# Kernel optimization log

Measured on AMD Instinct MI355X. Metric: run time of the kernel, lower is better.

Reference implementation:

```python
import jax, jax.numpy as jnp
import numpy as np

N = 50000   # nodes
E = 600000  # directed edges (self-loops added inside reference, per GCNConv default)
G = 64      # graphs in the batch
D = 128     # in_features
H = 128     # hidden_channels
C = 10      # num_classes


def setup_inputs() -> dict:
    key = jax.random.key(0)
    ks = jax.random.split(key, 9)
    x = jax.random.normal(ks[0], (N, D), dtype=jnp.float32)
    edge_index = jax.random.randint(ks[1], (2, E), 0, N, dtype=jnp.int64)
    batch = jnp.sort(jax.random.randint(ks[2], (N,), 0, G, dtype=jnp.int64))
    # GCNConv weights (glorot-ish scale) and biases; final linear layer
    W1 = jax.random.normal(ks[3], (D, H), dtype=jnp.float32) / np.sqrt(D).astype(np.float32)
    b1 = jnp.zeros((H,), dtype=jnp.float32)
    W2 = jax.random.normal(ks[4], (H, H), dtype=jnp.float32) / np.sqrt(H).astype(np.float32)
    b2 = jnp.zeros((H,), dtype=jnp.float32)
    Wlin = jax.random.normal(ks[5], (H, C), dtype=jnp.float32) / np.sqrt(H).astype(np.float32)
    blin = jnp.zeros((C,), dtype=jnp.float32)
    return {"x": x, "W1": W1, "b1": b1, "W2": W2, "b2": b2,
            "Wlin": Wlin, "blin": blin, "edge_index": edge_index, "batch": batch}


def _gcn_conv(x, W, b, row, col, norm):
    # x' = D^{-1/2}(A+I)D^{-1/2} (x W) + b ; aggregate messages from row (src) into col (dst)
    h = x @ W                                   # [N, H] dense GEMM
    msg = norm[:, None] * h[row]                # gather by source index [E+N, H]
    out = jax.ops.segment_sum(msg, col, num_segments=N)  # scatter-add to targets
    return out + b


def reference(x, W1, b1, W2, b2, Wlin, blin, edge_index, batch):
    loops = jnp.arange(N, dtype=edge_index.dtype)
    row = jnp.concatenate([edge_index[0], loops])   # sources (+ self loops)
    col = jnp.concatenate([edge_index[1], loops])   # targets (+ self loops)
    # symmetric degree normalization (degrees >= 1 thanks to self loops)
    deg = jax.ops.segment_sum(jnp.ones_like(col, dtype=jnp.float32), col, num_segments=N)
    dinv = jax.lax.rsqrt(deg)
    norm = dinv[row] * dinv[col]                    # [E+N]

    h = jax.nn.relu(_gcn_conv(x, W1, b1, row, col, norm))
    h = _gcn_conv(h, W2, b2, row, col, norm)

    # global mean pool over graphs
    sums = jax.ops.segment_sum(h, batch, num_segments=G)                       # [G, H]
    cnt = jax.ops.segment_sum(jnp.ones((N,), dtype=jnp.float32), batch, num_segments=G)
    pooled = sums / jnp.maximum(cnt, 1.0)[:, None]

    return pooled @ Wlin + blin                     # logits [G, C]
```

## Files before the change

kernel.cpp:

```cpp
#include <hip/hip_runtime.h>

#define NN 50000
#define NE 600000
#define NG 64
#define DIM 128
#define NCLS 10
#define SB 196
#define NNP 50176
#define KBLK 392
#define KCH 128
#define CAP 64
#define E2B ((NE / 2 + 255) / 256)
#define BSW_TAIL_START ((size_t)(NN >> 5) * 4096)

typedef unsigned short ushort;
typedef unsigned char uchar;
typedef __attribute__((ext_vector_type(8))) short short8;
typedef __attribute__((ext_vector_type(4))) float float4v;
typedef __attribute__((ext_vector_type(2))) float float2v;

__device__ __forceinline__ ushort f2bf(float f) {
    unsigned u = __float_as_uint(f);
    u += 0x7fff + ((u >> 16) & 1);
    return (ushort)(u >> 16);
}
__device__ __forceinline__ uchar f2fp8(float f) {
    int p = __builtin_amdgcn_cvt_pk_fp8_f32(f, f, 0, false);
    return (uchar)(p & 0xff);
}
__device__ __forceinline__ void accfp8(float* a, uint2 v) {
    float2v p0 = __builtin_amdgcn_cvt_pk_f32_fp8(v.x, false);
    float2v p1 = __builtin_amdgcn_cvt_pk_f32_fp8(v.x, true);
    float2v p2 = __builtin_amdgcn_cvt_pk_f32_fp8(v.y, false);
    float2v p3 = __builtin_amdgcn_cvt_pk_f32_fp8(v.y, true);
    a[0] += p0[0]; a[1] += p0[1]; a[2] += p1[0]; a[3] += p1[1];
    a[4] += p2[0]; a[5] += p2[1]; a[6] += p3[0]; a[7] += p3[1];
}

__global__ void k_init(int* __restrict__ cnt, const float* __restrict__ W1,
                       ushort* __restrict__ Wsw, float* __restrict__ T,
                       float* __restrict__ dinv, ushort* __restrict__ Bsw) {
    int b = blockIdx.x, t = threadIdx.x;
    if (b < SB) {
        int i = b * 256 + t;
        if (i < NN) cnt[i] = 0;
    } else if (b < SB + 64) {
        int tid = (b - SB) * 256 + t;
        int j = tid & 7;
        int lane = (tid >> 3) & 63;
        int frag = tid >> 9;
        int nt = frag >> 2, kc = frag & 3;
        int k = kc * 32 + (lane >> 4) * 8 + j;
        int n = nt * 16 + (lane & 15);
        Wsw[tid] = f2bf(W1[k * DIM + n]);
    } else if (b < SB + 64 + 784) {
        float4* w4 = (float4*)T;
        int base = (b - SB - 64) * 256 + t;
#pragma unroll
        for (int i = 0; i < 4; ++i)
            w4[base + i * 200704] = make_float4(0.f, 0.f, 0.f, 0.f);
    } else if (b == SB + 64 + 784) {
        if (t < NNP - NN) dinv[NN + t] = 0.f;
    } else {
        int idx = (b - (SB + 64 + 785)) * 256 + t;
        ((float4*)(Bsw + BSW_TAIL_START))[idx] = make_float4(0.f, 0.f, 0.f, 0.f);
    }
}

__global__ void k_fill(const int* __restrict__ row, const int* __restrict__ col,
                       int* __restrict__ cnt, ushort* __restrict__ ell) {
    int e = (blockIdx.x * blockDim.x + threadIdx.x) * 2;
    if (e < NE) {
        int2 r = *(const int2*)(row + e);
        int2 c = *(const int2*)(col + e);
        int p0 = atomicAdd(&cnt[c.x], 1);
        if (p0 < CAP) ell[(size_t)c.x * CAP + p0] = (ushort)r.x;
        int p1 = atomicAdd(&cnt[c.y], 1);
        if (p1 < CAP) ell[(size_t)c.y * CAP + p1] = (ushort)r.y;
    }
}

__global__ __launch_bounds__(256) void k_gemm_mfma(const float* __restrict__ Ain,
                                                   const ushort* __restrict__ Wsw,
                                                   const int* __restrict__ cnt,
                                                   uchar* __restrict__ Hs,
                                                   float* __restrict__ dinv) {
    const int t = threadIdx.x;
    const int wave = t >> 6, lane = t & 63;
    const int m = lane & 15, quad = lane >> 4;
    const int row0 = blockIdx.x * 64 + wave * 16;

    short8 bfrag[8][4];
#pragma unroll
    for (int nt = 0; nt < 8; ++nt)
#pragma unroll
        for (int kc = 0; kc < 4; ++kc)
            bfrag[nt][kc] = *(const short8*)(Wsw + ((nt * 4 + kc) * 64 + lane) * 8);

    float4v acc[8];
#pragma unroll
    for (int nt = 0; nt < 8; ++nt) acc[nt] = (float4v){0.f, 0.f, 0.f, 0.f};

    const int row = row0 + m;
    const int rclamp = row < NN ? row : NN - 1;

#pragma unroll
    for (int kc = 0; kc < 4; ++kc) {
        const float* ap = Ain + (size_t)rclamp * DIM + kc * 32 + quad * 8;
        float4 v0 = *(const float4*)ap;
        float4 v1 = *(const float4*)(ap + 4);
        union { short8 v; ushort u[8]; } tmp;
        tmp.u[0] = f2bf(v0.x); tmp.u[1] = f2bf(v0.y);
        tmp.u[2] = f2bf(v0.z); tmp.u[3] = f2bf(v0.w);
        tmp.u[4] = f2bf(v1.x); tmp.u[5] = f2bf(v1.y);
        tmp.u[6] = f2bf(v1.z); tmp.u[7] = f2bf(v1.w);
        short8 a = tmp.v;
#pragma unroll
        for (int nt = 0; nt < 8; ++nt)
            acc[nt] = __builtin_amdgcn_mfma_f32_16x16x32_bf16(a, bfrag[nt][kc], acc[nt], 0, 0, 0);
    }

#pragma unroll
    for (int reg = 0; reg < 4; ++reg) {
        int r = row0 + quad * 4 + reg;
        if (r < NN) {
            float d = rsqrtf(1.0f + (float)cnt[r]);
            if (m == 0) dinv[r] = d;
#pragma unroll
            for (int nt = 0; nt < 8; ++nt)
                Hs[(size_t)r * DIM + nt * 16 + m] = f2fp8(d * acc[nt][reg]);
        }
    }
}

__global__ __launch_bounds__(256) void k_gather_ell(const ushort* __restrict__ ell,
                                                    const int* __restrict__ deg,
                                                    const int* __restrict__ batch,
                                                    const float* __restrict__ bias,
                                                    const uchar* __restrict__ Hs,
                                                    float* __restrict__ T,
                                                    ushort* __restrict__ Bsw) {
    const int t = threadIdx.x, b = blockIdx.x;
    const int tn = t >> 4, lane = t & 15;
    const int node = b * 16 + tn;
    const ushort* rowp = ell + (size_t)node * CAP;
    int end = min(deg[node], CAP);
    const float d = rsqrtf(1.0f + (float)end);
    float* Trow = T + (size_t)batch[node] * NNP;
    const size_t off = (size_t)lane * 8;

    float a[8] = {0.f, 0.f, 0.f, 0.f, 0.f, 0.f, 0.f, 0.f};
    accfp8(a, *(const uint2*)(Hs + (size_t)node * DIM + off));
    if (lane == 0) atomicAdd(&Trow[node], d);

    int e = 0;
    for (; e + 8 <= end; e += 8) {
        uint4 iv = *(const uint4*)(rowp + e);
        int r0 = iv.x & 0xffff, r1 = iv.x >> 16;
        int r2 = iv.y & 0xffff, r3 = iv.y >> 16;
        int r4 = iv.z & 0xffff, r5 = iv.z >> 16;
        int r6 = iv.w & 0xffff, r7 = iv.w >> 16;
        if (lane < 8) atomicAdd(&Trow[rowp[e + lane]], d);
        uint2 v0 = *(const uint2*)(Hs + (size_t)r0 * DIM + off);
        uint2 v1 = *(const uint2*)(Hs + (size_t)r1 * DIM + off);
        uint2 v2 = *(const uint2*)(Hs + (size_t)r2 * DIM + off);
        uint2 v3 = *(const uint2*)(Hs + (size_t)r3 * DIM + off);
        uint2 v4 = *(const uint2*)(Hs + (size_t)r4 * DIM + off);
        uint2 v5 = *(const uint2*)(Hs + (size_t)r5 * DIM + off);
        uint2 v6 = *(const uint2*)(Hs + (size_t)r6 * DIM + off);
        uint2 v7 = *(const uint2*)(Hs + (size_t)r7 * DIM + off);
        accfp8(a, v0); accfp8(a, v1); accfp8(a, v2); accfp8(a, v3);
        accfp8(a, v4); accfp8(a, v5); accfp8(a, v6); accfp8(a, v7);
    }
    for (; e + 4 <= end; e += 4) {
        uint2 lv = *(const uint2*)(rowp + e);
        int r0 = lv.x & 0xffff, r1 = lv.x >> 16;
        int r2 = lv.y & 0xffff, r3 = lv.y >> 16;
        if (lane < 4) atomicAdd(&Trow[rowp[e + lane]], d);
        uint2 v0 = *(const uint2*)(Hs + (size_t)r0 * DIM + off);
        uint2 v1 = *(const uint2*)(Hs + (size_t)r1 * DIM + off);
        uint2 v2 = *(const uint2*)(Hs + (size_t)r2 * DIM + off);
        uint2 v3 = *(const uint2*)(Hs + (size_t)r3 * DIM + off);
        accfp8(a, v0); accfp8(a, v1); accfp8(a, v2); accfp8(a, v3);
    }
    for (; e < end; ++e) {
        int r = rowp[e];
        if (lane == 0) atomicAdd(&Trow[r], d);
        accfp8(a, *(const uint2*)(Hs + (size_t)r * DIM + off));
    }

    float4 b0 = *(const float4*)(bias + off);
    float4 b1 = *(const float4*)(bias + off + 4);
    a[0] = fmaxf(fmaf(a[0], d, b0.x), 0.f); a[1] = fmaxf(fmaf(a[1], d, b0.y), 0.f);
    a[2] = fmaxf(fmaf(a[2], d, b0.z), 0.f); a[3] = fmaxf(fmaf(a[3], d, b0.w), 0.f);
    a[4] = fmaxf(fmaf(a[4], d, b1.x), 0.f); a[5] = fmaxf(fmaf(a[5], d, b1.y), 0.f);
    a[6] = fmaxf(fmaf(a[6], d, b1.z), 0.f); a[7] = fmaxf(fmaf(a[7], d, b1.w), 0.f);

    __shared__ ushort Lb[16][128];
    union { short8 v; ushort u[8]; } st;
    st.u[0] = f2bf(a[0]); st.u[1] = f2bf(a[1]); st.u[2] = f2bf(a[2]); st.u[3] = f2bf(a[3]);
    st.u[4] = f2bf(a[4]); st.u[5] = f2bf(a[5]); st.u[6] = f2bf(a[6]); st.u[7] = f2bf(a[7]);
    *(short8*)(&Lb[tn][lane * 8]) = st.v;
    __syncthreads();

    const int nt = t >> 5, idx = t & 31;
    const int a_rel = (idx >> 4) & 1, fb = (idx >> 3) & 1, f7 = idx & 7;
    const int feat = nt * 16 + fb * 8 + f7;
    const int nl = a_rel * 8;
    uint4 o;
    o.x = (unsigned)Lb[nl + 0][feat] | ((unsigned)Lb[nl + 1][feat] << 16);
    o.y = (unsigned)Lb[nl + 2][feat] | ((unsigned)Lb[nl + 3][feat] << 16);
    o.z = (unsigned)Lb[nl + 4][feat] | ((unsigned)Lb[nl + 5][feat] << 16);
    o.w = (unsigned)Lb[nl + 6][feat] | ((unsigned)Lb[nl + 7][feat] << 16);
    size_t base = (size_t)(b >> 1) * 4096 + (size_t)nt * 512
                + (size_t)((b & 1) * 2 + a_rel) * 128 + (size_t)fb * 64 + (size_t)f7 * 8;
    *(uint4*)(Bsw + base) = o;
}

__global__ __launch_bounds__(256) void k_pool_gemm(const float* __restrict__ T,
                                                   const float* __restrict__ dinv,
                                                   const ushort* __restrict__ Bsw,
                                                   float* __restrict__ partial) {
    const int t = threadIdx.x;
    const int wave = t >> 6, lane = t & 63;
    const int m = lane & 15, quad = lane >> 4;
    const int g = wave * 16 + m;
    const int k0 = blockIdx.x * KCH;

    float4v acc[8];
#pragma unroll
    for (int nt = 0; nt < 8; ++nt) acc[nt] = (float4v){0.f, 0.f, 0.f, 0.f};

#pragma unroll
    for (int s = 0; s < KCH / 32; ++s) {
        const int kb = k0 + s * 32 + quad * 8;
        const float* ap = T + (size_t)g * NNP + kb;
        float4 a0 = *(const float4*)ap;
        float4 a1 = *(const float4*)(ap + 4);
        float4 d0 = *(const float4*)(dinv + kb);
        float4 d1 = *(const float4*)(dinv + kb + 4);
        union { short8 v; ushort u[8]; } af;
        af.u[0] = f2bf(a0.x * d0.x); af.u[1] = f2bf(a0.y * d0.y);
        af.u[2] = f2bf(a0.z * d0.z); af.u[3] = f2bf(a0.w * d0.w);
        af.u[4] = f2bf(a1.x * d1.x); af.u[5] = f2bf(a1.y * d1.y);
        af.u[6] = f2bf(a1.z * d1.z); af.u[7] = f2bf(a1.w * d1.w);

        const int t32 = (k0 >> 5) + s;
        const ushort* bb = Bsw + (size_t)t32 * 4096 + (size_t)lane * 8;
#pragma unroll
        for (int nt = 0; nt < 8; ++nt) {
            short8 bv = *(const short8*)(bb + nt * 512);
            acc[nt] = __builtin_amdgcn_mfma_f32_16x16x32_bf16(af.v, bv, acc[nt], 0, 0, 0);
        }
    }

    float* dst = partial + (size_t)blockIdx.x * (NG * DIM);
#pragma unroll
    for (int reg = 0; reg < 4; ++reg) {
        int gg = wave * 16 + quad * 4 + reg;
#pragma unroll
        for (int nt = 0; nt < 8; ++nt)
            dst[gg * DIM + nt * 16 + m] = acc[nt][reg];
    }
}

__global__ __launch_bounds__(512) void k_final(const float* __restrict__ partial,
                                               const float* __restrict__ W2,
                                               const float* __restrict__ b2,
                                               const float* __restrict__ Wlin,
                                               const float* __restrict__ blin,
                                               const int* __restrict__ batch,
                                               float* __restrict__ out) {
    const int g = blockIdx.x;
    const int t = threadIdx.x;
    const int c = t & 127, h = t >> 7;

    float s0 = 0.f, s1 = 0.f;
    const float* pp = partial + (size_t)h * 98 * (NG * DIM) + g * DIM + c;
#pragma unroll 7
    for (int i = 0; i < 98; i += 2) {
        s0 += pp[(size_t)i * (NG * DIM)];
        s1 += pp[(size_t)(i + 1) * (NG * DIM)];
    }

    __shared__ float red[512];
    __shared__ float Pl[DIM];
    __shared__ float pooled[DIM];
    red[t] = s0 + s1;
    __syncthreads();
    if (t < 128) Pl[t] = red[t] + red[t + 128] + red[t + 256] + red[t + 384];
    __syncthreads();
    if (t < 128) {
        float acc = 0.f;
        for (int k = 0; k < DIM; ++k) acc += Pl[k] * W2[k * DIM + t];
        int start;
        { int a = 0, bb = NN; while (a < bb) { int mm = (a + bb) >> 1; if (batch[mm] < g) a = mm + 1; else bb = mm; } start = a; }
        int endp;
        { int a = 0, bb = NN; while (a < bb) { int mm = (a + bb) >> 1; if (batch[mm] < g + 1) a = mm + 1; else bb = mm; } endp = a; }
        const int cnt = endp - start;
        pooled[t] = (cnt > 0) ? (acc / (float)cnt + b2[t]) : 0.f;
    }
    __syncthreads();
    if (t < NCLS) {
        float s2 = blin[t];
        for (int k = 0; k < DIM; ++k) s2 += pooled[k] * Wlin[k * NCLS + t];
        out[g * NCLS + t] = s2;
    }
}

extern "C" void kernel_launch(void* const* d_in, const int* in_sizes, int n_in,
                              void* d_out, int out_size, void* d_ws, size_t ws_size,
                              hipStream_t stream) {
    const float* x    = (const float*)d_in[0];
    const float* W1   = (const float*)d_in[1];
    const float* b1   = (const float*)d_in[2];
    const float* W2   = (const float*)d_in[3];
    const float* b2   = (const float*)d_in[4];
    const float* Wlin = (const float*)d_in[5];
    const float* blin = (const float*)d_in[6];
    const int* eidx   = (const int*)d_in[7];
    const int* batch  = (const int*)d_in[8];
    float* out = (float*)d_out;

    char* ws = (char*)d_ws;
    int*    cnt   = (int*)(ws + 0);
    float*  dinv  = (float*)(ws + 200000);
    ushort* Wsw   = (ushort*)(ws + 400704);
    ushort* ell   = (ushort*)(ws + 433472);
    uchar*  Hs1   = (uchar*)(ws + 6833472);
    float*  T     = (float*)(ws + 13233472);
    ushort* Bsw   = (ushort*)(ws + 26078528);
    float*  partial=(float*)(ws + 38923584);

    const int* erow = eidx;
    const int* ecol = eidx + NE;

    k_init<<<SB + 64 + 784 + 1 + 12, 256, 0, stream>>>(cnt, W1, Wsw, T, dinv, Bsw);
    k_fill<<<E2B, 256, 0, stream>>>(erow, ecol, cnt, ell);

    const int gemm_grid = (NN + 63) / 64;
    const int node_grid = NN / 16;

    k_gemm_mfma<<<gemm_grid, 256, 0, stream>>>(x, Wsw, cnt, Hs1, dinv);
    k_gather_ell<<<node_grid, 256, 0, stream>>>(ell, cnt, batch, b1, Hs1, T, Bsw);

    k_pool_gemm<<<KBLK, 256, 0, stream>>>(T, dinv, Bsw, partial);

    k_final<<<NG, 512, 0, stream>>>(partial, W2, b2, Wlin, blin, batch, out);
}
```

Measured before the change: 198.6 us.

## Count degrees early and overlap ELL fill with first-layer GEMM in one kernel

Degree counting moves into the init kernel, interleaved with zeroing T, so the GEMM can apply the dinv scaling without waiting for the ELL fill. The fill and GEMM are then merged into one launch whose blocks alternate roles, letting the atomic-heavy fill overlap the MFMA work. Alongside this, dinv scaling is folded into the gather epilogue so the pool GEMM no longer reads dinv, the gather loop is software-prefetched one batch of 8 neighbours ahead, and the final partial reduction is split into a separate atomic reduce kernel. The cost is an extra memset, a second counter array and one more kernel launch.

```diff
diff --git a/kernel.cpp b/kernel.cpp
--- a/kernel.cpp
+++ b/kernel.cpp
@@ -5,12 +5,15 @@
 #define NG 64
 #define DIM 128
 #define NCLS 10
-#define SB 196
 #define NNP 50176
 #define KBLK 392
 #define KCH 128
 #define CAP 64
-#define E2B ((NE / 2 + 255) / 256)
+#define FILLB 1172
+#define GEMMB 782
+#define PAIR (GEMMB * 2)
+#define TZB 784
+#define IPAIR (TZB * 2)
 #define BSW_TAIL_START ((size_t)(NN >> 5) * 4096)
 
 typedef unsigned short ushort;
@@ -36,16 +39,37 @@
     a[0] += p0[0]; a[1] += p0[1]; a[2] += p1[0]; a[3] += p1[1];
     a[4] += p2[0]; a[5] += p2[1]; a[6] += p3[0]; a[7] += p3[1];
 }
-
-__global__ void k_init(int* __restrict__ cnt, const float* __restrict__ W1,
-                       ushort* __restrict__ Wsw, float* __restrict__ T,
-                       float* __restrict__ dinv, ushort* __restrict__ Bsw) {
+__device__ __forceinline__ uint2 ldrow(const uchar* __restrict__ Hs, int r, size_t off) {
+    return *(const uint2*)(Hs + (size_t)r * DIM + off);
+}
+
+__global__ void k_init(const int* __restrict__ ecol, int* __restrict__ cnt,
+                       const float* __restrict__ W1, ushort* __restrict__ Wsw,
+                       float* __restrict__ T, ushort* __restrict__ Bsw,
+                       float* __restrict__ P) {
     int b = blockIdx.x, t = threadIdx.x;
-    if (b < SB) {
-        int i = b * 256 + t;
-        if (i < NN) cnt[i] = 0;
-    } else if (b < SB + 64) {
-        int tid = (b - SB) * 256 + t;
+    int role, id;
+    if (b < IPAIR)            { role = b & 1; id = b >> 1; }
+    else if (b < IPAIR + 388) { role = 1; id = TZB + (b - IPAIR); }
+    else if (b < IPAIR + 388 + 64) { role = 2; id = b - (IPAIR + 388); }
+    else if (b < IPAIR + 388 + 64 + 12) { role = 3; id = b - (IPAIR + 388 + 64); }
+    else { role = 4; id = b - (IPAIR + 388 + 64 + 12); }
+
+    if (role == 0) {
+        float4* w4 = (float4*)T;
+        int base = id * 256 + t;
+#pragma unroll
+        for (int i = 0; i < 4; ++i)
+            w4[base + i * 200704] = make_float4(0.f, 0.f, 0.f, 0.f);
+    } else if (role == 1) {
+        int e = (id * 256 + t) * 2;
+        if (e < NE) {
+            int2 c = *(const int2*)(ecol + e);
+            atomicAdd(&cnt[c.x], 1);
+            atomicAdd(&cnt[c.y], 1);
+        }
+    } else if (role == 2) {
+        int tid = id * 256 + t;
         int j = tid & 7;
         int lane = (tid >> 3) & 63;
         int frag = tid >> 9;
@@ -53,42 +77,44 @@
         int k = kc * 32 + (lane >> 4) * 8 + j;
         int n = nt * 16 + (lane & 15);
         Wsw[tid] = f2bf(W1[k * DIM + n]);
-    } else if (b < SB + 64 + 784) {
-        float4* w4 = (float4*)T;
-        int base = (b - SB - 64) * 256 + t;
-#pragma unroll
-        for (int i = 0; i < 4; ++i)
-            w4[base + i * 200704] = make_float4(0.f, 0.f, 0.f, 0.f);
-    } else if (b == SB + 64 + 784) {
-        if (t < NNP - NN) dinv[NN + t] = 0.f;
+    } else if (role == 3) {
+        int idx = id * 256 + t;
+        ((float4*)(Bsw + BSW_TAIL_START))[idx] = make_float4(0.f, 0.f, 0.f, 0.f);
     } else {
-        int idx = (b - (SB + 64 + 785)) * 256 + t;
-        ((float4*)(Bsw + BSW_TAIL_START))[idx] = make_float4(0.f, 0.f, 0.f, 0.f);
-    }
-}
-
-__global__ void k_fill(const int* __restrict__ row, const int* __restrict__ col,
-                       int* __restrict__ cnt, ushort* __restrict__ ell) {
-    int e = (blockIdx.x * blockDim.x + threadIdx.x) * 2;
-    if (e < NE) {
-        int2 r = *(const int2*)(row + e);
-        int2 c = *(const int2*)(col + e);
-        int p0 = atomicAdd(&cnt[c.x], 1);
-        if (p0 < CAP) ell[(size_t)c.x * CAP + p0] = (ushort)r.x;
-        int p1 = atomicAdd(&cnt[c.y], 1);
-        if (p1 < CAP) ell[(size_t)c.y * CAP + p1] = (ushort)r.y;
-    }
-}
-
-__global__ __launch_bounds__(256) void k_gemm_mfma(const float* __restrict__ Ain,
-                                                   const ushort* __restrict__ Wsw,
-                                                   const int* __restrict__ cnt,
-                                                   uchar* __restrict__ Hs,
-                                                   float* __restrict__ dinv) {
-    const int t = threadIdx.x;
+        int idx = id * 256 + t;
+        ((float4*)P)[idx] = make_float4(0.f, 0.f, 0.f, 0.f);
+    }
+}
+
+__global__ __launch_bounds__(256) void k_fillgemm(const int* __restrict__ erow,
+                                                  const int* __restrict__ ecol,
+                                                  int* __restrict__ cnt2,
+                                                  ushort* __restrict__ ell,
+                                                  const float* __restrict__ Ain,
+                                                  const ushort* __restrict__ Wsw,
+                                                  const int* __restrict__ cnt,
+                                                  uchar* __restrict__ Hs) {
+    const int b = blockIdx.x, t = threadIdx.x;
+    int role, id;
+    if (b < PAIR) { role = b & 1; id = b >> 1; }
+    else          { role = 0; id = GEMMB + (b - PAIR); }
+
+    if (role == 0) {
+        int e = (id * 256 + t) * 2;
+        if (e < NE) {
+            int2 r = *(const int2*)(erow + e);
+            int2 c = *(const int2*)(ecol + e);
+            int p0 = atomicAdd(&cnt2[c.x], 1);
+            if (p0 < CAP) ell[(size_t)c.x * CAP + p0] = (ushort)r.x;
+            int p1 = atomicAdd(&cnt2[c.y], 1);
+            if (p1 < CAP) ell[(size_t)c.y * CAP + p1] = (ushort)r.y;
+        }
+        return;
+    }
+
     const int wave = t >> 6, lane = t & 63;
     const int m = lane & 15, quad = lane >> 4;
-    const int row0 = blockIdx.x * 64 + wave * 16;
+    const int row0 = id * 64 + wave * 16;
 
     short8 bfrag[8][4];
 #pragma unroll
@@ -125,7 +151,6 @@
         int r = row0 + quad * 4 + reg;
         if (r < NN) {
             float d = rsqrtf(1.0f + (float)cnt[r]);
-            if (m == 0) dinv[r] = d;
 #pragma unroll
             for (int nt = 0; nt < 8; ++nt)
                 Hs[(size_t)r * DIM + nt * 16 + m] = f2fp8(d * acc[nt][reg]);
@@ -144,49 +169,54 @@
     const int tn = t >> 4, lane = t & 15;
     const int node = b * 16 + tn;
     const ushort* rowp = ell + (size_t)node * CAP;
-    int end = min(deg[node], CAP);
-    const float d = rsqrtf(1.0f + (float)end);
+    const int dg = deg[node];
+    const float d = rsqrtf(1.0f + (float)dg);
+    const int end = min(dg, CAP);
     float* Trow = T + (size_t)batch[node] * NNP;
     const size_t off = (size_t)lane * 8;
 
     float a[8] = {0.f, 0.f, 0.f, 0.f, 0.f, 0.f, 0.f, 0.f};
-    accfp8(a, *(const uint2*)(Hs + (size_t)node * DIM + off));
+    accfp8(a, ldrow(Hs, node, off));
     if (lane == 0) atomicAdd(&Trow[node], d);
 
     int e = 0;
-    for (; e + 8 <= end; e += 8) {
-        uint4 iv = *(const uint4*)(rowp + e);
-        int r0 = iv.x & 0xffff, r1 = iv.x >> 16;
-        int r2 = iv.y & 0xffff, r3 = iv.y >> 16;
-        int r4 = iv.z & 0xffff, r5 = iv.z >> 16;
-        int r6 = iv.w & 0xffff, r7 = iv.w >> 16;
+    if (end >= 8) {
+        uint4 iv = *(const uint4*)(rowp);
+        uint2 v0 = ldrow(Hs, iv.x & 0xffff, off), v1 = ldrow(Hs, iv.x >> 16, off);
+        uint2 v2 = ldrow(Hs, iv.y & 0xffff, off), v3 = ldrow(Hs, iv.y >> 16, off);
+        uint2 v4 = ldrow(Hs, iv.z & 0xffff, off), v5 = ldrow(Hs, iv.z >> 16, off);
+        uint2 v6 = ldrow(Hs, iv.w & 0xffff, off), v7 = ldrow(Hs, iv.w >> 16, off);
+        while (e + 16 <= end) {
+            uint4 ivn = *(const uint4*)(rowp + e + 8);
+            uint2 n0 = ldrow(Hs, ivn.x & 0xffff, off), n1 = ldrow(Hs, ivn.x >> 16, off);
+            uint2 n2 = ldrow(Hs, ivn.y & 0xffff, off), n3 = ldrow(Hs, ivn.y >> 16, off);
+            uint2 n4 = ldrow(Hs, ivn.z & 0xffff, off), n5 = ldrow(Hs, ivn.z >> 16, off);
+            uint2 n6 = ldrow(Hs, ivn.w & 0xffff, off), n7 = ldrow(Hs, ivn.w >> 16, off);
+            if (lane < 8) atomicAdd(&Trow[rowp[e + lane]], d);
+            accfp8(a, v0); accfp8(a, v1); accfp8(a, v2); accfp8(a, v3);
+            accfp8(a, v4); accfp8(a, v5); accfp8(a, v6); accfp8(a, v7);
+            v0 = n0; v1 = n1; v2 = n2; v3 = n3;
+            v4 = n4; v5 = n5; v6 = n6; v7 = n7;
+            e += 8;
+        }
         if (lane < 8) atomicAdd(&Trow[rowp[e + lane]], d);
-        uint2 v0 = *(const uint2*)(Hs + (size_t)r0 * DIM + off);
-        uint2 v1 = *(const uint2*)(Hs + (size_t)r1 * DIM + off);
-        uint2 v2 = *(const uint2*)(Hs + (size_t)r2 * DIM + off);
-        uint2 v3 = *(const uint2*)(Hs + (size_t)r3 * DIM + off);
-        uint2 v4 = *(const uint2*)(Hs + (size_t)r4 * DIM + off);
-        uint2 v5 = *(const uint2*)(Hs + (size_t)r5 * DIM + off);
-        uint2 v6 = *(const uint2*)(Hs + (size_t)r6 * DIM + off);
-        uint2 v7 = *(const uint2*)(Hs + (size_t)r7 * DIM + off);
         accfp8(a, v0); accfp8(a, v1); accfp8(a, v2); accfp8(a, v3);
         accfp8(a, v4); accfp8(a, v5); accfp8(a, v6); accfp8(a, v7);
+        e += 8;
     }
     for (; e + 4 <= end; e += 4) {
         uint2 lv = *(const uint2*)(rowp + e);
         int r0 = lv.x & 0xffff, r1 = lv.x >> 16;
         int r2 = lv.y & 0xffff, r3 = lv.y >> 16;
         if (lane < 4) atomicAdd(&Trow[rowp[e + lane]], d);
-        uint2 v0 = *(const uint2*)(Hs + (size_t)r0 * DIM + off);
-        uint2 v1 = *(const uint2*)(Hs + (size_t)r1 * DIM + off);
-        uint2 v2 = *(const uint2*)(Hs + (size_t)r2 * DIM + off);
-        uint2 v3 = *(const uint2*)(Hs + (size_t)r3 * DIM + off);
-        accfp8(a, v0); accfp8(a, v1); accfp8(a, v2); accfp8(a, v3);
+        uint2 w0 = ldrow(Hs, r0, off), w1 = ldrow(Hs, r1, off);
+        uint2 w2 = ldrow(Hs, r2, off), w3 = ldrow(Hs, r3, off);
+        accfp8(a, w0); accfp8(a, w1); accfp8(a, w2); accfp8(a, w3);
     }
     for (; e < end; ++e) {
         int r = rowp[e];
         if (lane == 0) atomicAdd(&Trow[r], d);
-        accfp8(a, *(const uint2*)(Hs + (size_t)r * DIM + off));
+        accfp8(a, ldrow(Hs, r, off));
     }
 
     float4 b0 = *(const float4*)(bias + off);
@@ -198,8 +228,10 @@
 
     __shared__ ushort Lb[16][128];
     union { short8 v; ushort u[8]; } st;
-    st.u[0] = f2bf(a[0]); st.u[1] = f2bf(a[1]); st.u[2] = f2bf(a[2]); st.u[3] = f2bf(a[3]);
-    st.u[4] = f2bf(a[4]); st.u[5] = f2bf(a[5]); st.u[6] = f2bf(a[6]); st.u[7] = f2bf(a[7]);
+    st.u[0] = f2bf(d * a[0]); st.u[1] = f2bf(d * a[1]);
+    st.u[2] = f2bf(d * a[2]); st.u[3] = f2bf(d * a[3]);
+    st.u[4] = f2bf(d * a[4]); st.u[5] = f2bf(d * a[5]);
+    st.u[6] = f2bf(d * a[6]); st.u[7] = f2bf(d * a[7]);
     *(short8*)(&Lb[tn][lane * 8]) = st.v;
     __syncthreads();
 
@@ -218,7 +250,6 @@
 }
 
 __global__ __launch_bounds__(256) void k_pool_gemm(const float* __restrict__ T,
-                                                   const float* __restrict__ dinv,
                                                    const ushort* __restrict__ Bsw,
                                                    float* __restrict__ partial) {
     const int t = threadIdx.x;
@@ -237,13 +268,11 @@
         const float* ap = T + (size_t)g * NNP + kb;
         float4 a0 = *(const float4*)ap;
         float4 a1 = *(const float4*)(ap + 4);
-        float4 d0 = *(const float4*)(dinv + kb);
-        float4 d1 = *(const float4*)(dinv + kb + 4);
         union { short8 v; ushort u[8]; } af;
-        af.u[0] = f2bf(a0.x * d0.x); af.u[1] = f2bf(a0.y * d0.y);
-        af.u[2] = f2bf(a0.z * d0.z); af.u[3] = f2bf(a0.w * d0.w);
-        af.u[4] = f2bf(a1.x * d1.x); af.u[5] = f2bf(a1.y * d1.y);
-        af.u[6] = f2bf(a1.z * d1.z); af.u[7] = f2bf(a1.w * d1.w);
+        af.u[0] = f2bf(a0.x); af.u[1] = f2bf(a0.y);
+        af.u[2] = f2bf(a0.z); af.u[3] = f2bf(a0.w);
+        af.u[4] = f2bf(a1.x); af.u[5] = f2bf(a1.y);
+        af.u[6] = f2bf(a1.z); af.u[7] = f2bf(a1.w);
 
         const int t32 = (k0 >> 5) + s;
         const ushort* bb = Bsw + (size_t)t32 * 4096 + (size_t)lane * 8;
@@ -264,7 +293,18 @@
     }
 }
 
-__global__ __launch_bounds__(512) void k_final(const float* __restrict__ partial,
+__global__ __launch_bounds__(256) void k_red(const float* __restrict__ partial,
+                                             float* __restrict__ P) {
+    int tid = blockIdx.x * 256 + threadIdx.x;
+    int elem = tid & 8191, h = tid >> 13;
+    const float* pp = partial + (size_t)h * 49 * (NG * DIM) + elem;
+    float s = 0.f;
+#pragma unroll
+    for (int i = 0; i < 49; ++i) s += pp[(size_t)i * (NG * DIM)];
+    atomicAdd(&P[elem], s);
+}
+
+__global__ __launch_bounds__(128) void k_final(const float* __restrict__ P,
                                                const float* __restrict__ W2,
                                                const float* __restrict__ b2,
                                                const float* __restrict__ Wlin,
@@ -273,33 +313,19 @@
                                                float* __restrict__ out) {
     const int g = blockIdx.x;
     const int t = threadIdx.x;
-    const int c = t & 127, h = t >> 7;
-
-    float s0 = 0.f, s1 = 0.f;
-    const float* pp = partial + (size_t)h * 98 * (NG * DIM) + g * DIM + c;
-#pragma unroll 7
-    for (int i = 0; i < 98; i += 2) {
-        s0 += pp[(size_t)i * (NG * DIM)];
-        s1 += pp[(size_t)(i + 1) * (NG * DIM)];
-    }
-
-    __shared__ float red[512];
+    int start;
+    { int a = 0, bb = NN; while (a < bb) { int mm = (a + bb) >> 1; if (batch[mm] < g) a = mm + 1; else bb = mm; } start = a; }
+    int endp;
+    { int a = 0, bb = NN; while (a < bb) { int mm = (a + bb) >> 1; if (batch[mm] < g + 1) a = mm + 1; else bb = mm; } endp = a; }
+    const int cnt = endp - start;
+
     __shared__ float Pl[DIM];
     __shared__ float pooled[DIM];
-    red[t] = s0 + s1;
+    Pl[t] = P[g * DIM + t];
     __syncthreads();
-    if (t < 128) Pl[t] = red[t] + red[t + 128] + red[t + 256] + red[t + 384];
-    __syncthreads();
-    if (t < 128) {
-        float acc = 0.f;
-        for (int k = 0; k < DIM; ++k) acc += Pl[k] * W2[k * DIM + t];
-        int start;
-        { int a = 0, bb = NN; while (a < bb) { int mm = (a + bb) >> 1; if (batch[mm] < g) a = mm + 1; else bb = mm; } start = a; }
-        int endp;
-        { int a = 0, bb = NN; while (a < bb) { int mm = (a + bb) >> 1; if (batch[mm] < g + 1) a = mm + 1; else bb = mm; } endp = a; }
-        const int cnt = endp - start;
-        pooled[t] = (cnt > 0) ? (acc / (float)cnt + b2[t]) : 0.f;
-    }
+    float acc = 0.f;
+    for (int k = 0; k < DIM; ++k) acc += Pl[k] * W2[k * DIM + t];
+    pooled[t] = (cnt > 0) ? (acc / (float)cnt + b2[t]) : 0.f;
     __syncthreads();
     if (t < NCLS) {
         float s2 = blin[t];
@@ -324,27 +350,28 @@
 
     char* ws = (char*)d_ws;
     int*    cnt   = (int*)(ws + 0);
-    float*  dinv  = (float*)(ws + 200000);
-    ushort* Wsw   = (ushort*)(ws + 400704);
+    int*    cnt2  = (int*)(ws + 200000);
+    ushort* Wsw   = (ushort*)(ws + 400000);
     ushort* ell   = (ushort*)(ws + 433472);
     uchar*  Hs1   = (uchar*)(ws + 6833472);
     float*  T     = (float*)(ws + 13233472);
     ushort* Bsw   = (ushort*)(ws + 26078528);
     float*  partial=(float*)(ws + 38923584);
+    float*  P     = (float*)(ws + 51768640);
 
     const int* erow = eidx;
     const int* ecol = eidx + NE;
 
-    k_init<<<SB + 64 + 784 + 1 + 12, 256, 0, stream>>>(cnt, W1, Wsw, T, dinv, Bsw);
-    k_fill<<<E2B, 256, 0, stream>>>(erow, ecol, cnt, ell);
-
-    const int gemm_grid = (NN + 63) / 64;
-    const int node_grid = NN / 16;
-
-    k_gemm_mfma<<<gemm_grid, 256, 0, stream>>>(x, Wsw, cnt, Hs1, dinv);
-    k_gather_ell<<<node_grid, 256, 0, stream>>>(ell, cnt, batch, b1, Hs1, T, Bsw);
-
-    k_pool_gemm<<<KBLK, 256, 0, stream>>>(T, dinv, Bsw, partial);
-
-    k_final<<<NG, 512, 0, stream>>>(partial, W2, b2, Wlin, blin, batch, out);
-}
+    hipMemsetAsync(ws, 0, 400000, stream);
+    k_init<<<IPAIR + 388 + 64 + 12 + 8, 256, 0, stream>>>(ecol, cnt, W1, Wsw, T, Bsw, P);
+
+    k_fillgemm<<<PAIR + (FILLB - GEMMB), 256, 0, stream>>>(erow, ecol, cnt2, ell,
+                                                           x, Wsw, cnt, Hs1);
+
+    k_gather_ell<<<NN / 16, 256, 0, stream>>>(ell, cnt, batch, b1, Hs1, T, Bsw);
+
+    k_pool_gemm<<<KBLK, 256, 0, stream>>>(T, Bsw, partial);
+    k_red<<<256, 256, 0, stream>>>(partial, P);
+
+    k_final<<<NG, 128, 0, stream>>>(P, W2, b2, Wlin, blin, batch, out);
+}
```

Measured after the change: 213.6 us. 1.08x slower.
